# Kernel optimization log

Measured on AMD Instinct MI355X. Metric: run time of the kernel, lower is better.

Reference implementation:

```python
import jax, jax.numpy as jnp
import numpy as np

B, TQ, TK, D, V = 16, 64, 512, 256, 32000


def setup_inputs() -> dict:
    key = jax.random.key(0)
    k = jax.random.split(key, 8)
    return {
        "domainslots": jax.random.normal(k[0], (B, TQ, D), jnp.float32),
        "out_states": jax.random.normal(k[1], (B, TQ, D), jnp.float32),
        "context": jax.random.normal(k[2], (B, TK, D), jnp.float32),
        "context_plain": jax.random.randint(k[3], (B, TK), 0, V, jnp.int64 if jax.config.jax_enable_x64 else jnp.int32),
        "W_state": jax.random.normal(k[4], (D, V), jnp.float32) * 0.02,
        "b_state": jnp.zeros((V,), jnp.float32),
        "W_gen": jax.random.normal(k[5], (3 * D, 1), jnp.float32) * 0.02,
        "b_gen": jnp.zeros((1,), jnp.float32),
    }


def reference(domainslots, out_states, context, context_plain, W_state, b_state, W_gen, b_gen):
    d = out_states.shape[-1]
    # pointer attention: softmax(Q K^T / sqrt(d)) over context  -> [B, TQ, TK]
    scores = jnp.einsum("bqd,bkd->bqk", out_states, context) / jnp.sqrt(jnp.asarray(d, out_states.dtype))
    pointer_attn = jax.nn.softmax(scores, axis=-1)

    # generation distribution over vocab  -> [B, TQ, V]
    p_state_vocab = jax.nn.softmax(out_states @ W_state + b_state, axis=-1)

    # copy distribution: scatter-add attention mass onto source token ids
    b_idx = jnp.arange(B)[:, None, None]           # [B,1,1]
    q_idx = jnp.arange(TQ)[None, :, None]          # [1,TQ,1]
    v_idx = context_plain[:, None, :]              # [B,1,TK] broadcast over TQ
    p_state_ptr = jnp.zeros((B, TQ, V), p_state_vocab.dtype).at[b_idx, q_idx, v_idx].add(pointer_attn)

    # attention-weighted context vector  -> [B, TQ, D]
    context_vec = jnp.einsum("bqk,bkd->bqd", pointer_attn, context)

    # generation gate  -> [B, TQ, 1]
    p_gen_vec = jnp.concatenate([out_states, context_vec, domainslots], axis=-1)
    p_state_gen = jax.nn.sigmoid(p_gen_vec @ W_gen + b_gen)

    p_state_out = p_state_gen * p_state_vocab + (1.0 - p_state_gen) * p_state_ptr
    return jnp.log(p_state_out)
```

## Files before the change

kernel.cpp:

```cpp
#include <hip/hip_runtime.h>
#include <math.h>

typedef short short8 __attribute__((ext_vector_type(8)));
typedef float f32x4 __attribute__((ext_vector_type(4)));

#define B_ 16
#define TQ_ 64
#define TK_ 512
#define D_ 256
#define V_ 32000
#define M_ (B_ * TQ_)

__device__ __forceinline__ unsigned short f2bf(float x) {
    unsigned int u = __float_as_uint(x);
    unsigned int r = (u + 0x7fffu + ((u >> 16) & 1u)) >> 16;
    return (unsigned short)r;
}

__device__ __forceinline__ void gload_lds16(const void* g, void* l) {
    __builtin_amdgcn_global_load_lds(
        (const __attribute__((address_space(1))) void*)g,
        (__attribute__((address_space(3))) void*)l, 16, 0, 0);
}

__global__ __launch_bounds__(256) void dedup_kernel(
    const int* __restrict__ cp, int* __restrict__ nexta, int* __restrict__ leader)
{
    __shared__ __align__(16) int c[TK_];
    const int b = blockIdx.x, tid = threadIdx.x;
    c[tid] = cp[b * TK_ + tid];
    c[tid + 256] = cp[b * TK_ + 256 + tid];
    __syncthreads();
    for (int k = tid; k < TK_; k += 256) {
        const int v = c[k];
        int fm = 1024, nx = 1024;
#pragma unroll 8
        for (int j0 = 0; j0 < TK_; j0 += 4) {
            const int4 q = *(const int4*)&c[j0];
            if (q.x == v) { fm = min(fm, j0);     if (j0     > k) nx = min(nx, j0);     }
            if (q.y == v) { fm = min(fm, j0 + 1); if (j0 + 1 > k) nx = min(nx, j0 + 1); }
            if (q.z == v) { fm = min(fm, j0 + 2); if (j0 + 2 > k) nx = min(nx, j0 + 2); }
            if (q.w == v) { fm = min(fm, j0 + 3); if (j0 + 3 > k) nx = min(nx, j0 + 3); }
        }
        nexta[b * TK_ + k] = (nx < 1024) ? nx : -1;
        leader[b * TK_ + k] = (fm == k) ? 1 : 0;
    }
}

__global__ __launch_bounds__(256) void conv_a_kernel(
    const float* __restrict__ A, unsigned short* __restrict__ Ab)
{
    const int i = (blockIdx.x * 256 + threadIdx.x) * 4;
    const float4 v = *(const float4*)&A[i];
    ushort4 o;
    o.x = f2bf(v.x); o.y = f2bf(v.y); o.z = f2bf(v.z); o.w = f2bf(v.w);
    *(ushort4*)&Ab[i] = o;
}

__global__ __launch_bounds__(256) void conv_w_kernel(
    const float* __restrict__ W, unsigned short* __restrict__ Wt)
{
    __shared__ float tile[64][65];
    const int tid = threadIdx.x;
    const int k0 = (blockIdx.x & 3) * 64;
    const int n0 = (blockIdx.x >> 2) * 64;
#pragma unroll
    for (int i = 0; i < 16; i++) {
        const int r = i * 4 + (tid >> 6), cc = tid & 63;
        tile[r][cc] = W[(k0 + r) * V_ + n0 + cc];
    }
    __syncthreads();
#pragma unroll
    for (int i = 0; i < 4; i++) {
        const int nl = i * 16 + (tid >> 4);
        const int kq = (tid & 15) * 4;
        ushort4 o;
        o.x = f2bf(tile[kq + 0][nl]);
        o.y = f2bf(tile[kq + 1][nl]);
        o.z = f2bf(tile[kq + 2][nl]);
        o.w = f2bf(tile[kq + 3][nl]);
        *(ushort4*)&Wt[(n0 + nl) * D_ + k0 + kq] = o;
    }
}

__global__ __launch_bounds__(256) void conv_c_kernel(
    const float* __restrict__ ctx, unsigned short* __restrict__ Cb,
    unsigned short* __restrict__ Ct)
{
    __shared__ float tile[64][65];
    const int tid = threadIdx.x;
    const int b = blockIdx.x >> 5;
    const int r5 = blockIdx.x & 31;
    const int k0 = (r5 >> 2) * 64;
    const int d0 = (r5 & 3) * 64;
#pragma unroll
    for (int i = 0; i < 16; i++) {
        const int r = i * 4 + (tid >> 6), cc = tid & 63;
        const float v = ctx[((b * TK_) + k0 + r) * D_ + d0 + cc];
        tile[r][cc] = v;
        Cb[((b * TK_) + k0 + r) * D_ + d0 + cc] = f2bf(v);
    }
    __syncthreads();
#pragma unroll
    for (int i = 0; i < 4; i++) {
        const int dl = i * 16 + (tid >> 4);
        const int kq = (tid & 15) * 4;
        ushort4 o;
        o.x = f2bf(tile[kq + 0][dl]);
        o.y = f2bf(tile[kq + 1][dl]);
        o.z = f2bf(tile[kq + 2][dl]);
        o.w = f2bf(tile[kq + 3][dl]);
        *(ushort4*)&Ct[((b * D_) + d0 + dl) * TK_ + k0 + kq] = o;
    }
}

template <int LDA, int LDB, int KTOT>
__global__ __launch_bounds__(256) void gemm_small(
    const unsigned short* __restrict__ A,
    const unsigned short* __restrict__ Bt,
    float* __restrict__ C, int ldc, int nchunks, int btrows, float scale)
{
    __shared__ short Al[64][72];
    __shared__ short Bl[128][72];
    const int tid = threadIdx.x;
    const int b = blockIdx.x / nchunks;
    const int n0 = (blockIdx.x % nchunks) * 128;
    A += (size_t)b * 64 * LDA;
    Bt += (size_t)b * btrows * LDB;
    C += (size_t)b * 64 * ldc;

    const int wid = tid >> 6;
    const int lane = tid & 63;
    const int wm = wid & 1, wn = wid >> 1;
    const int quad = lane >> 4, l15 = lane & 15;

    f32x4 acc[2][4];
#pragma unroll
    for (int i = 0; i < 2; i++)
#pragma unroll
        for (int j = 0; j < 4; j++) acc[i][j] = f32x4{0.f, 0.f, 0.f, 0.f};

    for (int k0 = 0; k0 < KTOT; k0 += 64) {
        __syncthreads();
#pragma unroll
        for (int i = 0; i < 2; i++) {
            const int c = tid + i * 256;
            const int r = c >> 3, kc = (c & 7) * 8;
            *(uint4*)&Al[r][kc] = *(const uint4*)&A[r * LDA + k0 + kc];
        }
#pragma unroll
        for (int i = 0; i < 4; i++) {
            const int c = tid + i * 256;
            const int r = c >> 3, kc = (c & 7) * 8;
            *(uint4*)&Bl[r][kc] = *(const uint4*)&Bt[(n0 + r) * LDB + k0 + kc];
        }
        __syncthreads();
#pragma unroll
        for (int ks = 0; ks < 64; ks += 32) {
            short8 af[2], bf[4];
#pragma unroll
            for (int mt = 0; mt < 2; mt++)
                af[mt] = *(const short8*)&Al[wm * 32 + mt * 16 + l15][ks + quad * 8];
#pragma unroll
            for (int nt = 0; nt < 4; nt++)
                bf[nt] = *(const short8*)&Bl[wn * 64 + nt * 16 + l15][ks + quad * 8];
#pragma unroll
            for (int mt = 0; mt < 2; mt++)
#pragma unroll
                for (int nt = 0; nt < 4; nt++)
                    acc[mt][nt] = __builtin_amdgcn_mfma_f32_16x16x32_bf16(
                        af[mt], bf[nt], acc[mt][nt], 0, 0, 0);
        }
    }
#pragma unroll
    for (int mt = 0; mt < 2; mt++)
#pragma unroll
        for (int nt = 0; nt < 4; nt++)
#pragma unroll
            for (int r = 0; r < 4; r++) {
                const int rl = wm * 32 + mt * 16 + quad * 4 + r;
                const int col = n0 + wn * 64 + nt * 16 + l15;
                C[rl * ldc + col] = acc[mt][nt][r] * scale;
            }
}

__global__ __launch_bounds__(256) void softmax_kernel(
    float* __restrict__ S, unsigned short* __restrict__ Pb)
{
    const int w = threadIdx.x >> 6, lane = threadIdx.x & 63;
    const int row = blockIdx.x * 4 + w;
    float v[8], m = -1e30f;
#pragma unroll
    for (int j = 0; j < 8; j++) { v[j] = S[row * TK_ + lane + 64 * j]; m = fmaxf(m, v[j]); }
#pragma unroll
    for (int off = 32; off; off >>= 1) m = fmaxf(m, __shfl_xor(m, off));
    float s = 0.f;
#pragma unroll
    for (int j = 0; j < 8; j++) { v[j] = __expf(v[j] - m); s += v[j]; }
#pragma unroll
    for (int off = 32; off; off >>= 1) s += __shfl_xor(s, off);
    const float inv = 1.0f / s;
#pragma unroll
    for (int j = 0; j < 8; j++) {
        const float p = v[j] * inv;
        S[row * TK_ + lane + 64 * j] = p;
        Pb[row * TK_ + lane + 64 * j] = f2bf(p);
    }
}

__global__ __launch_bounds__(256) void pgen_kernel(
    const float* __restrict__ os, const float* __restrict__ cv,
    const float* __restrict__ dm, const float* __restrict__ W_gen,
    const float* __restrict__ b_gen, float* __restrict__ pg)
{
    const int w = threadIdx.x >> 6, lane = threadIdx.x & 63;
    const int row = blockIdx.x * 4 + w;
    const int d4 = lane * 4;
    const float4 o4 = *(const float4*)&os[row * D_ + d4];
    const float4 c4 = *(const float4*)&cv[row * D_ + d4];
    const float4 m4 = *(const float4*)&dm[row * D_ + d4];
    const float4 w0 = *(const float4*)&W_gen[d4];
    const float4 w1 = *(const float4*)&W_gen[D_ + d4];
    const float4 w2 = *(const float4*)&W_gen[2 * D_ + d4];
    float p = o4.x * w0.x + o4.y * w0.y + o4.z * w0.z + o4.w * w0.w
            + c4.x * w1.x + c4.y * w1.y + c4.z * w1.z + c4.w * w1.w
            + m4.x * w2.x + m4.y * w2.y + m4.z * w2.z + m4.w * w2.w;
#pragma unroll
    for (int off = 32; off; off >>= 1) p += __shfl_xor(p, off);
    if (lane == 0) pg[row] = 1.0f / (1.0f + __expf(-(p + b_gen[0])));
}

__global__ __launch_bounds__(256) void gemm_vocab_fused(
    const unsigned short* __restrict__ A,
    const unsigned short* __restrict__ Bt,
    const float* __restrict__ b_state,
    float* __restrict__ Z,
    float* __restrict__ out)
{
    __shared__ short Al[128][64];
    __shared__ short Bl[128][64];
    __shared__ float bst[128];

    const int tid = threadIdx.x;
    const int bx = blockIdx.x;
    const int m0 = (bx & 7) * 128;
    const int n0 = (bx >> 3) * 128;

    if (tid < 128) bst[tid] = b_state[n0 + tid];

    const int wid = tid >> 6, lane = tid & 63;
    const int wm = wid & 1, wn = wid >> 1;
    const int quad = lane >> 4, l15 = lane & 15;
    const int srow = lane >> 3;
    const int scol = (lane & 7) * 8;

    f32x4 acc[4][4];
#pragma unroll
    for (int i = 0; i < 4; i++)
#pragma unroll
        for (int j = 0; j < 4; j++) acc[i][j] = f32x4{0.f, 0.f, 0.f, 0.f};

    for (int k0 = 0; k0 < D_; k0 += 64) {
        __syncthreads();
#pragma unroll
        for (int j = 0; j < 4; j++) {
            const int c = j * 4 + wid;
            const int r = c * 8 + srow;
            gload_lds16(&A[(size_t)(m0 + r) * D_ + k0 + scol], &Al[c * 8][0]);
        }
#pragma unroll
        for (int j = 0; j < 4; j++) {
            const int c = j * 4 + wid;
            const int r = c * 8 + srow;
            gload_lds16(&Bt[(size_t)(n0 + r) * D_ + k0 + scol], &Bl[c * 8][0]);
        }
        __syncthreads();
#pragma unroll
        for (int ks = 0; ks < 64; ks += 32) {
            short8 af[4], bf[4];
#pragma unroll
            for (int mt = 0; mt < 4; mt++)
                af[mt] = *(const short8*)&Al[wm * 64 + mt * 16 + l15][ks + quad * 8];
#pragma unroll
            for (int nt = 0; nt < 4; nt++)
                bf[nt] = *(const short8*)&Bl[wn * 64 + nt * 16 + l15][ks + quad * 8];
#pragma unroll
            for (int mt = 0; mt < 4; mt++)
#pragma unroll
                for (int nt = 0; nt < 4; nt++)
                    acc[mt][nt] = __builtin_amdgcn_mfma_f32_16x16x32_bf16(
                        af[mt], bf[nt], acc[mt][nt], 0, 0, 0);
        }
    }

#pragma unroll
    for (int mt = 0; mt < 4; mt++) {
        float rs[4] = {0.f, 0.f, 0.f, 0.f};
#pragma unroll
        for (int nt = 0; nt < 4; nt++) {
            const float bcol = bst[wn * 64 + nt * 16 + l15];
#pragma unroll
            for (int r = 0; r < 4; r++) {
                const int row = wm * 64 + mt * 16 + quad * 4 + r;
                const int col = wn * 64 + nt * 16 + l15;
                const float v = acc[mt][nt][r] + bcol;
                out[(size_t)(m0 + row) * V_ + n0 + col] = v;
                rs[r] += __expf(v);
            }
        }
#pragma unroll
        for (int r = 0; r < 4; r++) {
            float v = rs[r];
            v += __shfl_xor(v, 1);
            v += __shfl_xor(v, 2);
            v += __shfl_xor(v, 4);
            v += __shfl_xor(v, 8);
            if (l15 == 0)
                atomicAdd(&Z[m0 + wm * 64 + mt * 16 + quad * 4 + r], v);
        }
    }
}

__global__ __launch_bounds__(256) void rowconst_kernel(
    const float* __restrict__ pg, const float* __restrict__ Z, float* __restrict__ rc)
{
    const int r = blockIdx.x * 256 + threadIdx.x;
    rc[r] = logf(pg[r]) - logf(Z[r]);
}

__global__ __launch_bounds__(256) void epilogue_kernel(
    const float* __restrict__ rc, float* __restrict__ out)
{
    const int row = blockIdx.x;
    const float r = rc[row];
    float4* p = (float4*)(out + (size_t)row * V_);
    for (int i = threadIdx.x; i < V_ / 4; i += 256) {
        float4 v = p[i];
        v.x += r; v.y += r; v.z += r; v.w += r;
        p[i] = v;
    }
}

__global__ __launch_bounds__(256) void fixup_kernel(
    const int* __restrict__ cp, const int* __restrict__ nexta,
    const int* __restrict__ leader, const float* __restrict__ attn,
    const float* __restrict__ pg, float* __restrict__ out)
{
    const int t = blockIdx.x * 256 + threadIdx.x;
    const int row = t >> 9, k = t & 511;
    const int b = row >> 6;
    if (!leader[b * TK_ + k]) return;
    float a = attn[row * TK_ + k];
    int j = nexta[b * TK_ + k];
    while (j >= 0) { a += attn[row * TK_ + j]; j = nexta[b * TK_ + j]; }
    const float val = (1.0f - pg[row]) * a;
    const int v = cp[b * TK_ + k];
    const size_t idx = (size_t)row * V_ + v;
    out[idx] = logf(expf(out[idx]) + val);
}

extern "C" void kernel_launch(void* const* d_in, const int* in_sizes, int n_in,
                              void* d_out, int out_size, void* d_ws, size_t ws_size,
                              hipStream_t stream)
{
    const float* domainslots = (const float*)d_in[0];
    const float* out_states  = (const float*)d_in[1];
    const float* context     = (const float*)d_in[2];
    const int*   cp          = (const int*)d_in[3];
    const float* W_state     = (const float*)d_in[4];
    const float* b_state     = (const float*)d_in[5];
    const float* W_gen       = (const float*)d_in[6];
    const float* b_gen       = (const float*)d_in[7];
    float* out = (float*)d_out;
    char* ws = (char*)d_ws;

    float* Z      = (float*)(ws);
    float* pg     = (float*)(ws + 4096);
    float* rc     = (float*)(ws + 8192);
    float* S      = (float*)(ws + 12288);
    int* nexta    = (int*)(ws + 2109440);
    int* leader   = (int*)(ws + 2142208);
    unsigned short* Ab = (unsigned short*)(ws + 2174976);
    unsigned short* Wt = (unsigned short*)(ws + 2699264);
    unsigned short* Cb = (unsigned short*)(ws + 19083264);
    unsigned short* Ct = (unsigned short*)(ws + 23277568);
    unsigned short* Pb = (unsigned short*)(ws + 27471872);
    float* cv     = (float*)(ws + 28520448);

    hipMemsetAsync(Z, 0, M_ * sizeof(float), stream);
    dedup_kernel<<<B_, 256, 0, stream>>>(cp, nexta, leader);
    conv_a_kernel<<<(M_ * D_) / 1024, 256, 0, stream>>>(out_states, Ab);
    conv_w_kernel<<<(D_ / 64) * (V_ / 64), 256, 0, stream>>>(W_state, Wt);
    conv_c_kernel<<<B_ * 32, 256, 0, stream>>>(context, Cb, Ct);

    gemm_small<D_, D_, D_><<<B_ * 4, 256, 0, stream>>>(Ab, Cb, S, TK_, 4, TK_, 0.0625f);
    softmax_kernel<<<M_ / 4, 256, 0, stream>>>(S, Pb);
    gemm_small<TK_, TK_, TK_><<<B_ * 2, 256, 0, stream>>>(Pb, Ct, cv, D_, 2, D_, 1.0f);
    pgen_kernel<<<M_ / 4, 256, 0, stream>>>(out_states, cv, domainslots, W_gen, b_gen, pg);

    gemm_vocab_fused<<<(M_ / 128) * (V_ / 128), 256, 0, stream>>>(Ab, Wt, b_state, Z, out);
    rowconst_kernel<<<M_ / 256, 256, 0, stream>>>(pg, Z, rc);
    epilogue_kernel<<<M_, 256, 0, stream>>>(rc, out);
    fixup_kernel<<<(M_ * TK_) / 256, 256, 0, stream>>>(cp, nexta, leader, S, pg, out);
}
```

Before: 349.1 us.

## Fuse epilogues, stage bf16 logits, swizzle vocab GEMM LDS, retile small GEMMs

The vocab GEMM can now write bf16 logits to a workspace buffer, and a single fused epilogue turns them into fp32 log-probs and applies the pointer-copy fixup in one row pass. This replaces the old rowconst, epilogue and fixup kernels and the fp32 read-modify-write of the output. The vocab GEMM LDS layout is XOR-swizzled to avoid bank conflicts. The QK GEMM converts context to bf16 on the fly instead of reading a separate copy, the small GEMMs use 64-wide tiles for more blocks, and dedup is split across twice as many blocks. Storing logits in bf16 before the final add lowers output precision, and the bf16 path only runs if the workspace is large enough.

```diff
diff --git a/kernel.cpp b/kernel.cpp
--- a/kernel.cpp
+++ b/kernel.cpp
@@ -16,6 +16,9 @@
     unsigned int r = (u + 0x7fffu + ((u >> 16) & 1u)) >> 16;
     return (unsigned short)r;
 }
+__device__ __forceinline__ float bf2f(unsigned short u) {
+    return __uint_as_float((unsigned int)u << 16);
+}
 
 __device__ __forceinline__ void gload_lds16(const void* g, void* l) {
     __builtin_amdgcn_global_load_lds(
@@ -27,24 +30,23 @@
     const int* __restrict__ cp, int* __restrict__ nexta, int* __restrict__ leader)
 {
     __shared__ __align__(16) int c[TK_];
-    const int b = blockIdx.x, tid = threadIdx.x;
+    const int b = blockIdx.x >> 1, half = blockIdx.x & 1, tid = threadIdx.x;
     c[tid] = cp[b * TK_ + tid];
     c[tid + 256] = cp[b * TK_ + 256 + tid];
     __syncthreads();
-    for (int k = tid; k < TK_; k += 256) {
-        const int v = c[k];
-        int fm = 1024, nx = 1024;
+    const int k = half * 256 + tid;
+    const int v = c[k];
+    int fm = 1024, nx = 1024;
 #pragma unroll 8
-        for (int j0 = 0; j0 < TK_; j0 += 4) {
-            const int4 q = *(const int4*)&c[j0];
-            if (q.x == v) { fm = min(fm, j0);     if (j0     > k) nx = min(nx, j0);     }
-            if (q.y == v) { fm = min(fm, j0 + 1); if (j0 + 1 > k) nx = min(nx, j0 + 1); }
-            if (q.z == v) { fm = min(fm, j0 + 2); if (j0 + 2 > k) nx = min(nx, j0 + 2); }
-            if (q.w == v) { fm = min(fm, j0 + 3); if (j0 + 3 > k) nx = min(nx, j0 + 3); }
-        }
-        nexta[b * TK_ + k] = (nx < 1024) ? nx : -1;
-        leader[b * TK_ + k] = (fm == k) ? 1 : 0;
-    }
+    for (int j0 = 0; j0 < TK_; j0 += 4) {
+        const int4 q = *(const int4*)&c[j0];
+        if (q.x == v) { fm = min(fm, j0);     if (j0     > k) nx = min(nx, j0);     }
+        if (q.y == v) { fm = min(fm, j0 + 1); if (j0 + 1 > k) nx = min(nx, j0 + 1); }
+        if (q.z == v) { fm = min(fm, j0 + 2); if (j0 + 2 > k) nx = min(nx, j0 + 2); }
+        if (q.w == v) { fm = min(fm, j0 + 3); if (j0 + 3 > k) nx = min(nx, j0 + 3); }
+    }
+    nexta[b * TK_ + k] = (nx < 1024) ? nx : -1;
+    leader[b * TK_ + k] = (fm == k) ? 1 : 0;
 }
 
 __global__ __launch_bounds__(256) void conv_a_kernel(
@@ -83,9 +85,8 @@
     }
 }
 
-__global__ __launch_bounds__(256) void conv_c_kernel(
-    const float* __restrict__ ctx, unsigned short* __restrict__ Cb,
-    unsigned short* __restrict__ Ct)
+__global__ __launch_bounds__(256) void conv_ct_kernel(
+    const float* __restrict__ ctx, unsigned short* __restrict__ Ct)
 {
     __shared__ float tile[64][65];
     const int tid = threadIdx.x;
@@ -96,9 +97,7 @@
 #pragma unroll
     for (int i = 0; i < 16; i++) {
         const int r = i * 4 + (tid >> 6), cc = tid & 63;
-        const float v = ctx[((b * TK_) + k0 + r) * D_ + d0 + cc];
-        tile[r][cc] = v;
-        Cb[((b * TK_) + k0 + r) * D_ + d0 + cc] = f2bf(v);
+        tile[r][cc] = ctx[((b * TK_) + k0 + r) * D_ + d0 + cc];
     }
     __syncthreads();
 #pragma unroll
@@ -114,60 +113,60 @@
     }
 }
 
-template <int LDA, int LDB, int KTOT>
-__global__ __launch_bounds__(256) void gemm_small(
-    const unsigned short* __restrict__ A,
-    const unsigned short* __restrict__ Bt,
-    float* __restrict__ C, int ldc, int nchunks, int btrows, float scale)
+__global__ __launch_bounds__(256) void gemm_qk(
+    const unsigned short* __restrict__ Ab, const float* __restrict__ ctx,
+    float* __restrict__ S)
 {
     __shared__ short Al[64][72];
-    __shared__ short Bl[128][72];
+    __shared__ short Bl[64][72];
     const int tid = threadIdx.x;
-    const int b = blockIdx.x / nchunks;
-    const int n0 = (blockIdx.x % nchunks) * 128;
-    A += (size_t)b * 64 * LDA;
-    Bt += (size_t)b * btrows * LDB;
-    C += (size_t)b * 64 * ldc;
-
-    const int wid = tid >> 6;
-    const int lane = tid & 63;
+    const int b = blockIdx.x >> 3;
+    const int n0 = (blockIdx.x & 7) * 64;
+    const unsigned short* A = Ab + (size_t)b * 64 * D_;
+    const float* Bt = ctx + (size_t)b * TK_ * D_;
+    float* C = S + (size_t)b * 64 * TK_;
+
+    const int wid = tid >> 6, lane = tid & 63;
     const int wm = wid & 1, wn = wid >> 1;
     const int quad = lane >> 4, l15 = lane & 15;
 
-    f32x4 acc[2][4];
+    f32x4 acc[2][2];
 #pragma unroll
     for (int i = 0; i < 2; i++)
 #pragma unroll
-        for (int j = 0; j < 4; j++) acc[i][j] = f32x4{0.f, 0.f, 0.f, 0.f};
-
-    for (int k0 = 0; k0 < KTOT; k0 += 64) {
+        for (int j = 0; j < 2; j++) acc[i][j] = f32x4{0.f, 0.f, 0.f, 0.f};
+
+    for (int k0 = 0; k0 < D_; k0 += 64) {
         __syncthreads();
 #pragma unroll
         for (int i = 0; i < 2; i++) {
             const int c = tid + i * 256;
             const int r = c >> 3, kc = (c & 7) * 8;
-            *(uint4*)&Al[r][kc] = *(const uint4*)&A[r * LDA + k0 + kc];
+            *(uint4*)&Al[r][kc] = *(const uint4*)&A[r * D_ + k0 + kc];
         }
 #pragma unroll
         for (int i = 0; i < 4; i++) {
             const int c = tid + i * 256;
-            const int r = c >> 3, kc = (c & 7) * 8;
-            *(uint4*)&Bl[r][kc] = *(const uint4*)&Bt[(n0 + r) * LDB + k0 + kc];
+            const int r = c >> 4, kc = (c & 15) * 4;
+            const float4 v = *(const float4*)&Bt[(size_t)(n0 + r) * D_ + k0 + kc];
+            ushort4 o;
+            o.x = f2bf(v.x); o.y = f2bf(v.y); o.z = f2bf(v.z); o.w = f2bf(v.w);
+            *(ushort4*)&Bl[r][kc] = o;
         }
         __syncthreads();
 #pragma unroll
         for (int ks = 0; ks < 64; ks += 32) {
-            short8 af[2], bf[4];
+            short8 af[2], bf[2];
 #pragma unroll
             for (int mt = 0; mt < 2; mt++)
                 af[mt] = *(const short8*)&Al[wm * 32 + mt * 16 + l15][ks + quad * 8];
 #pragma unroll
-            for (int nt = 0; nt < 4; nt++)
-                bf[nt] = *(const short8*)&Bl[wn * 64 + nt * 16 + l15][ks + quad * 8];
+            for (int nt = 0; nt < 2; nt++)
+                bf[nt] = *(const short8*)&Bl[wn * 32 + nt * 16 + l15][ks + quad * 8];
 #pragma unroll
             for (int mt = 0; mt < 2; mt++)
 #pragma unroll
-                for (int nt = 0; nt < 4; nt++)
+                for (int nt = 0; nt < 2; nt++)
                     acc[mt][nt] = __builtin_amdgcn_mfma_f32_16x16x32_bf16(
                         af[mt], bf[nt], acc[mt][nt], 0, 0, 0);
         }
@@ -175,12 +174,79 @@
 #pragma unroll
     for (int mt = 0; mt < 2; mt++)
 #pragma unroll
-        for (int nt = 0; nt < 4; nt++)
+        for (int nt = 0; nt < 2; nt++)
 #pragma unroll
             for (int r = 0; r < 4; r++) {
                 const int rl = wm * 32 + mt * 16 + quad * 4 + r;
-                const int col = n0 + wn * 64 + nt * 16 + l15;
-                C[rl * ldc + col] = acc[mt][nt][r] * scale;
+                const int col = n0 + wn * 32 + nt * 16 + l15;
+                C[rl * TK_ + col] = acc[mt][nt][r] * 0.0625f;
+            }
+}
+
+__global__ __launch_bounds__(256) void gemm_pv(
+    const unsigned short* __restrict__ Pb, const unsigned short* __restrict__ Ctg,
+    float* __restrict__ cv)
+{
+    __shared__ short Al[64][72];
+    __shared__ short Bl[64][72];
+    const int tid = threadIdx.x;
+    const int b = blockIdx.x >> 2;
+    const int n0 = (blockIdx.x & 3) * 64;
+    const unsigned short* A = Pb + (size_t)b * 64 * TK_;
+    const unsigned short* Bt = Ctg + (size_t)b * D_ * TK_;
+    float* C = cv + (size_t)b * 64 * D_;
+
+    const int wid = tid >> 6, lane = tid & 63;
+    const int wm = wid & 1, wn = wid >> 1;
+    const int quad = lane >> 4, l15 = lane & 15;
+
+    f32x4 acc[2][2];
+#pragma unroll
+    for (int i = 0; i < 2; i++)
+#pragma unroll
+        for (int j = 0; j < 2; j++) acc[i][j] = f32x4{0.f, 0.f, 0.f, 0.f};
+
+    for (int k0 = 0; k0 < TK_; k0 += 64) {
+        __syncthreads();
+#pragma unroll
+        for (int i = 0; i < 2; i++) {
+            const int c = tid + i * 256;
+            const int r = c >> 3, kc = (c & 7) * 8;
+            *(uint4*)&Al[r][kc] = *(const uint4*)&A[(size_t)r * TK_ + k0 + kc];
+        }
+#pragma unroll
+        for (int i = 0; i < 2; i++) {
+            const int c = tid + i * 256;
+            const int r = c >> 3, kc = (c & 7) * 8;
+            *(uint4*)&Bl[r][kc] = *(const uint4*)&Bt[(size_t)(n0 + r) * TK_ + k0 + kc];
+        }
+        __syncthreads();
+#pragma unroll
+        for (int ks = 0; ks < 64; ks += 32) {
+            short8 af[2], bf[2];
+#pragma unroll
+            for (int mt = 0; mt < 2; mt++)
+                af[mt] = *(const short8*)&Al[wm * 32 + mt * 16 + l15][ks + quad * 8];
+#pragma unroll
+            for (int nt = 0; nt < 2; nt++)
+                bf[nt] = *(const short8*)&Bl[wn * 32 + nt * 16 + l15][ks + quad * 8];
+#pragma unroll
+            for (int mt = 0; mt < 2; mt++)
+#pragma unroll
+                for (int nt = 0; nt < 2; nt++)
+                    acc[mt][nt] = __builtin_amdgcn_mfma_f32_16x16x32_bf16(
+                        af[mt], bf[nt], acc[mt][nt], 0, 0, 0);
+        }
+    }
+#pragma unroll
+    for (int mt = 0; mt < 2; mt++)
+#pragma unroll
+        for (int nt = 0; nt < 2; nt++)
+#pragma unroll
+            for (int r = 0; r < 4; r++) {
+                const int rl = wm * 32 + mt * 16 + quad * 4 + r;
+                const int col = n0 + wn * 32 + nt * 16 + l15;
+                C[rl * D_ + col] = acc[mt][nt][r];
             }
 }
 
@@ -230,12 +296,14 @@
     if (lane == 0) pg[row] = 1.0f / (1.0f + __expf(-(p + b_gen[0])));
 }
 
+template <int BF16>
 __global__ __launch_bounds__(256) void gemm_vocab_fused(
     const unsigned short* __restrict__ A,
     const unsigned short* __restrict__ Bt,
     const float* __restrict__ b_state,
     float* __restrict__ Z,
-    float* __restrict__ out)
+    unsigned short* __restrict__ Lb,
+    float* __restrict__ Fout)
 {
     __shared__ short Al[128][64];
     __shared__ short Bl[128][64];
@@ -251,8 +319,7 @@
     const int wid = tid >> 6, lane = tid & 63;
     const int wm = wid & 1, wn = wid >> 1;
     const int quad = lane >> 4, l15 = lane & 15;
-    const int srow = lane >> 3;
-    const int scol = (lane & 7) * 8;
+    const int h = l15 & 7;
 
     f32x4 acc[4][4];
 #pragma unroll
@@ -263,27 +330,36 @@
     for (int k0 = 0; k0 < D_; k0 += 64) {
         __syncthreads();
 #pragma unroll
-        for (int j = 0; j < 4; j++) {
-            const int c = j * 4 + wid;
-            const int r = c * 8 + srow;
-            gload_lds16(&A[(size_t)(m0 + r) * D_ + k0 + scol], &Al[c * 8][0]);
-        }
-#pragma unroll
-        for (int j = 0; j < 4; j++) {
-            const int c = j * 4 + wid;
-            const int r = c * 8 + srow;
-            gload_lds16(&Bt[(size_t)(n0 + r) * D_ + k0 + scol], &Bl[c * 8][0]);
+        for (int i = 0; i < 4; i++) {
+            const int cid = (i * 4 + wid) * 64 + lane;
+            const int r = cid >> 3;
+            const int clog = (cid & 7) ^ (r & 7);
+            gload_lds16(&A[(size_t)(m0 + r) * D_ + k0 + clog * 8],
+                        &Al[0][0] + (i * 4 + wid) * 512);
+        }
+#pragma unroll
+        for (int i = 0; i < 4; i++) {
+            const int cid = (i * 4 + wid) * 64 + lane;
+            const int r = cid >> 3;
+            const int clog = (cid & 7) ^ (r & 7);
+            gload_lds16(&Bt[(size_t)(n0 + r) * D_ + k0 + clog * 8],
+                        &Bl[0][0] + (i * 4 + wid) * 512);
         }
         __syncthreads();
 #pragma unroll
         for (int ks = 0; ks < 64; ks += 32) {
+            const int cbase = ks >> 3;
             short8 af[4], bf[4];
 #pragma unroll
-            for (int mt = 0; mt < 4; mt++)
-                af[mt] = *(const short8*)&Al[wm * 64 + mt * 16 + l15][ks + quad * 8];
-#pragma unroll
-            for (int nt = 0; nt < 4; nt++)
-                bf[nt] = *(const short8*)&Bl[wn * 64 + nt * 16 + l15][ks + quad * 8];
+            for (int mt = 0; mt < 4; mt++) {
+                const int pc = (cbase + quad) ^ h;
+                af[mt] = *(const short8*)&Al[wm * 64 + mt * 16 + l15][pc * 8];
+            }
+#pragma unroll
+            for (int nt = 0; nt < 4; nt++) {
+                const int pc = (cbase + quad) ^ h;
+                bf[nt] = *(const short8*)&Bl[wn * 64 + nt * 16 + l15][pc * 8];
+            }
 #pragma unroll
             for (int mt = 0; mt < 4; mt++)
 #pragma unroll
@@ -304,7 +380,10 @@
                 const int row = wm * 64 + mt * 16 + quad * 4 + r;
                 const int col = wn * 64 + nt * 16 + l15;
                 const float v = acc[mt][nt][r] + bcol;
-                out[(size_t)(m0 + row) * V_ + n0 + col] = v;
+                if (BF16)
+                    Lb[(size_t)(m0 + row) * V_ + n0 + col] = f2bf(v);
+                else
+                    Fout[(size_t)(m0 + row) * V_ + n0 + col] = v;
                 rs[r] += __expf(v);
             }
         }
@@ -321,42 +400,52 @@
     }
 }
 
-__global__ __launch_bounds__(256) void rowconst_kernel(
-    const float* __restrict__ pg, const float* __restrict__ Z, float* __restrict__ rc)
-{
-    const int r = blockIdx.x * 256 + threadIdx.x;
-    rc[r] = logf(pg[r]) - logf(Z[r]);
-}
-
-__global__ __launch_bounds__(256) void epilogue_kernel(
-    const float* __restrict__ rc, float* __restrict__ out)
-{
-    const int row = blockIdx.x;
-    const float r = rc[row];
-    float4* p = (float4*)(out + (size_t)row * V_);
-    for (int i = threadIdx.x; i < V_ / 4; i += 256) {
-        float4 v = p[i];
-        v.x += r; v.y += r; v.z += r; v.w += r;
-        p[i] = v;
-    }
-}
-
-__global__ __launch_bounds__(256) void fixup_kernel(
+template <int BF16>
+__global__ __launch_bounds__(256) void epilogue_fused(
+    const unsigned short* __restrict__ Lb,
+    const float* __restrict__ pg, const float* __restrict__ Z,
     const int* __restrict__ cp, const int* __restrict__ nexta,
     const int* __restrict__ leader, const float* __restrict__ attn,
-    const float* __restrict__ pg, float* __restrict__ out)
-{
-    const int t = blockIdx.x * 256 + threadIdx.x;
-    const int row = t >> 9, k = t & 511;
+    float* __restrict__ out)
+{
+    const int row = blockIdx.x, tid = threadIdx.x;
+    const float pgr = pg[row];
+    const float rc = logf(pgr) - logf(Z[row]);
+    float* orow = out + (size_t)row * V_;
+    if (BF16) {
+        const unsigned short* lrow = Lb + (size_t)row * V_;
+        for (int i = tid; i < V_ / 8; i += 256) {
+            const ushort4 u0 = *(const ushort4*)&lrow[i * 8];
+            const ushort4 u1 = *(const ushort4*)&lrow[i * 8 + 4];
+            float4 f0, f1;
+            f0.x = bf2f(u0.x) + rc; f0.y = bf2f(u0.y) + rc;
+            f0.z = bf2f(u0.z) + rc; f0.w = bf2f(u0.w) + rc;
+            f1.x = bf2f(u1.x) + rc; f1.y = bf2f(u1.y) + rc;
+            f1.z = bf2f(u1.z) + rc; f1.w = bf2f(u1.w) + rc;
+            *(float4*)&orow[i * 8] = f0;
+            *(float4*)&orow[i * 8 + 4] = f1;
+        }
+    } else {
+        for (int i = tid; i < V_ / 4; i += 256) {
+            float4 v = *(float4*)&orow[i * 4];
+            v.x += rc; v.y += rc; v.z += rc; v.w += rc;
+            *(float4*)&orow[i * 4] = v;
+        }
+    }
+    __syncthreads();
     const int b = row >> 6;
-    if (!leader[b * TK_ + k]) return;
-    float a = attn[row * TK_ + k];
-    int j = nexta[b * TK_ + k];
-    while (j >= 0) { a += attn[row * TK_ + j]; j = nexta[b * TK_ + j]; }
-    const float val = (1.0f - pg[row]) * a;
-    const int v = cp[b * TK_ + k];
-    const size_t idx = (size_t)row * V_ + v;
-    out[idx] = logf(expf(out[idx]) + val);
+    for (int k = tid; k < TK_; k += 256) {
+        if (!leader[b * TK_ + k]) continue;
+        float a = attn[(size_t)row * TK_ + k];
+        int j = nexta[b * TK_ + k];
+        while (j >= 0) { a += attn[(size_t)row * TK_ + j]; j = nexta[b * TK_ + j]; }
+        const float val = (1.0f - pgr) * a;
+        const int v = cp[b * TK_ + k];
+        float base;
+        if (BF16) base = bf2f(Lb[(size_t)row * V_ + v]) + rc;
+        else      base = orow[v];
+        orow[v] = logf(__expf(base) + val);
+    }
 }
 
 extern "C" void kernel_launch(void* const* d_in, const int* in_sizes, int n_in,
@@ -376,30 +465,35 @@
 
     float* Z      = (float*)(ws);
     float* pg     = (float*)(ws + 4096);
-    float* rc     = (float*)(ws + 8192);
-    float* S      = (float*)(ws + 12288);
-    int* nexta    = (int*)(ws + 2109440);
-    int* leader   = (int*)(ws + 2142208);
-    unsigned short* Ab = (unsigned short*)(ws + 2174976);
-    unsigned short* Wt = (unsigned short*)(ws + 2699264);
-    unsigned short* Cb = (unsigned short*)(ws + 19083264);
-    unsigned short* Ct = (unsigned short*)(ws + 23277568);
-    unsigned short* Pb = (unsigned short*)(ws + 27471872);
-    float* cv     = (float*)(ws + 28520448);
+    float* S      = (float*)(ws + 8192);
+    int* nexta    = (int*)(ws + 2105344);
+    int* leader   = (int*)(ws + 2138112);
+    unsigned short* Ab = (unsigned short*)(ws + 2170880);
+    unsigned short* Wt = (unsigned short*)(ws + 2695168);
+    unsigned short* Ct = (unsigned short*)(ws + 19079168);
+    unsigned short* Pb = (unsigned short*)(ws + 23273472);
+    float* cv     = (float*)(ws + 24322048);
+    unsigned short* Lb = (unsigned short*)(ws + 25370624);
+    const bool use_lb = (ws_size >= (size_t)90906624);
 
     hipMemsetAsync(Z, 0, M_ * sizeof(float), stream);
-    dedup_kernel<<<B_, 256, 0, stream>>>(cp, nexta, leader);
+    dedup_kernel<<<B_ * 2, 256, 0, stream>>>(cp, nexta, leader);
     conv_a_kernel<<<(M_ * D_) / 1024, 256, 0, stream>>>(out_states, Ab);
     conv_w_kernel<<<(D_ / 64) * (V_ / 64), 256, 0, stream>>>(W_state, Wt);
-    conv_c_kernel<<<B_ * 32, 256, 0, stream>>>(context, Cb, Ct);
-
-    gemm_small<D_, D_, D_><<<B_ * 4, 256, 0, stream>>>(Ab, Cb, S, TK_, 4, TK_, 0.0625f);
+    conv_ct_kernel<<<B_ * 32, 256, 0, stream>>>(context, Ct);
+
+    gemm_qk<<<B_ * 8, 256, 0, stream>>>(Ab, context, S);
     softmax_kernel<<<M_ / 4, 256, 0, stream>>>(S, Pb);
-    gemm_small<TK_, TK_, TK_><<<B_ * 2, 256, 0, stream>>>(Pb, Ct, cv, D_, 2, D_, 1.0f);
+    gemm_pv<<<B_ * 4, 256, 0, stream>>>(Pb, Ct, cv);
     pgen_kernel<<<M_ / 4, 256, 0, stream>>>(out_states, cv, domainslots, W_gen, b_gen, pg);
 
-    gemm_vocab_fused<<<(M_ / 128) * (V_ / 128), 256, 0, stream>>>(Ab, Wt, b_state, Z, out);
-    rowconst_kernel<<<M_ / 256, 256, 0, stream>>>(pg, Z, rc);
-    epilogue_kernel<<<M_, 256, 0, stream>>>(rc, out);
-    fixup_kernel<<<(M_ * TK_) / 256, 256, 0, stream>>>(cp, nexta, leader, S, pg, out);
-}
+    if (use_lb) {
+        gemm_vocab_fused<1><<<(M_ / 128) * (V_ / 128), 256, 0, stream>>>(
+            Ab, Wt, b_state, Z, Lb, out);
+        epilogue_fused<1><<<M_, 256, 0, stream>>>(Lb, pg, Z, cp, nexta, leader, S, out);
+    } else {
+        gemm_vocab_fused<0><<<(M_ / 128) * (V_ / 128), 256, 0, stream>>>(
+            Ab, Wt, b_state, Z, Lb, out);
+        epilogue_fused<0><<<M_, 256, 0, stream>>>(Lb, pg, Z, cp, nexta, leader, S, out);
+    }
+}
```

Result: slower. 389.5 us (+11.6%).
